# Kernel optimization log

Hardware: AMD Instinct MI355X
Metric: run time of the kernel (lower is better)

The kernel has to match this reference:

```python
import jax, jax.numpy as jnp
import numpy as np

EPS_CB = 1e-6   # ConvBlock norm_layer eps
EPS_LVC = 1e-5  # default BatchNorm2d/1d eps in LVC branch


def _conv(x, w, stride=1, pad=0):
    return jax.lax.conv_general_dilated(
        x, w, (stride, stride), [(pad, pad), (pad, pad)],
        dimension_numbers=("NCHW", "OIHW", "NCHW"))


def _bn2d(x, g, b, eps):
    # inference-style BN with running_mean=0, running_var=1
    inv = 1.0 / jnp.sqrt(1.0 + eps)
    return x * (g * inv)[None, :, None, None] + b[None, :, None, None]


def setup_inputs() -> dict:
    key = jax.random.key(0)
    ks = jax.random.split(key, 24)
    B, C, Cm, K, H, W = 32, 512, 128, 64, 32, 32
    rn = lambda k, s, sc=0.05: jax.random.normal(k, s, dtype=jnp.float32) * sc
    std = 1.0 / (K * C) ** 0.5
    return {
        "x": jax.random.normal(ks[0], (B, C, H, W), dtype=jnp.float32),
        "c1_w": rn(ks[1], (Cm, C, 1, 1)),
        "bn1_g": 1.0 + rn(ks[2], (Cm,)), "bn1_b": rn(ks[3], (Cm,)),
        "c2_w": rn(ks[4], (Cm, Cm, 3, 3)),
        "bn2_g": 1.0 + rn(ks[5], (Cm,)), "bn2_b": rn(ks[6], (Cm,)),
        "c3_w": rn(ks[7], (C, Cm, 1, 1)),
        "bn3_g": 1.0 + rn(ks[8], (C,)), "bn3_b": rn(ks[9], (C,)),
        "rc_w": rn(ks[10], (C, C, 1, 1)),
        "rbn_g": 1.0 + rn(ks[11], (C,)), "rbn_b": rn(ks[12], (C,)),
        "lvc_w": rn(ks[13], (C, C, 1, 1)),
        "lvcbn_g": 1.0 + rn(ks[14], (C,)), "lvcbn_b": rn(ks[15], (C,)),
        "codewords": jax.random.uniform(ks[16], (K, C), minval=-std, maxval=std, dtype=jnp.float32),
        "scale": jax.random.uniform(ks[17], (K,), minval=-1.0, maxval=0.0, dtype=jnp.float32),
        "enbn_g": 1.0 + rn(ks[18], (K,)), "enbn_b": rn(ks[19], (K,)),
        "fc_w": rn(ks[20], (C, C)), "fc_b": rn(ks[21], (C,)),
    }


def reference(x, c1_w, bn1_g, bn1_b, c2_w, bn2_g, bn2_b, c3_w, bn3_g, bn3_b,
              rc_w, rbn_g, rbn_b, lvc_w, lvcbn_g, lvcbn_b,
              codewords, scale, enbn_g, enbn_b, fc_w, fc_b):
    # ---- ConvBlock (ResNet bottleneck with residual 1x1 conv) ----
    h = jax.nn.relu(_bn2d(_conv(x, c1_w), bn1_g, bn1_b, EPS_CB))
    h = jax.nn.relu(_bn2d(_conv(h, c2_w, pad=1), bn2_g, bn2_b, EPS_CB))
    h = _bn2d(_conv(h, c3_w), bn3_g, bn3_b, EPS_CB)
    r = _bn2d(_conv(x, rc_w), rbn_g, rbn_b, EPS_CB)
    xb = jax.nn.relu(h + r)  # (B,C,H,W)

    # ---- LVC: 1x1 conv + BN + ReLU, then Encoding ----
    e = jax.nn.relu(_bn2d(_conv(xb, lvc_w), lvcbn_g, lvcbn_b, EPS_LVC))
    B, C, H, W = e.shape
    ef = e.reshape(B, C, H * W).transpose(0, 2, 1)  # (B,N,C)

    x2 = jnp.sum(ef * ef, axis=-1)                       # (B,N)
    c2 = jnp.sum(codewords * codewords, axis=-1)         # (K,)
    xc = jnp.einsum("bnc,kc->bnk", ef, codewords)        # (B,N,K)
    sl2 = scale[None, None, :] * (x2[:, :, None] - 2.0 * xc + c2[None, None, :])
    a = jax.nn.softmax(sl2, axis=2)                      # (B,N,K)

    # aggregate: sum_n a_{nk} (x_n - c_k)
    enc = jnp.einsum("bnk,bnc->bkc", a, ef) \
          - jnp.sum(a, axis=1)[:, :, None] * codewords[None, :, :]  # (B,K,C)

    # BatchNorm1d over the K (channel) axis, inference-style, then ReLU
    inv = 1.0 / jnp.sqrt(1.0 + EPS_LVC)
    enc = jax.nn.relu(enc * (enbn_g * inv)[None, :, None] + enbn_b[None, :, None])
    en = jnp.mean(enc, axis=1)                           # (B,C)

    # ---- SE-style gating ----
    gam = jax.nn.sigmoid(en @ fc_w.T + fc_b)             # (B,C)
    return jax.nn.relu(xb + xb * gam[:, :, None, None])
```

## Files before the change

### kernel.cpp

```cpp
#include <hip/hip_runtime.h>
#include <math.h>

constexpr int BATCH = 32;
constexpr int C     = 512;
constexpr int CM    = 128;
constexpr int KW    = 64;
constexpr int NPIX  = 1024;

typedef unsigned short u16;
typedef __attribute__((ext_vector_type(8))) short bf16x8;
typedef __attribute__((ext_vector_type(4))) float f32x4;
typedef __attribute__((ext_vector_type(8))) unsigned short u16x8;

__device__ __forceinline__ float bf2f(u16 u) {
    unsigned int v = ((unsigned int)u) << 16;
    return __uint_as_float(v);
}
__device__ __forceinline__ u16 f2bf(float f) {
    unsigned int u = __float_as_uint(f);
    u = u + 0x7FFFu + ((u >> 16) & 1u);
    return (u16)(u >> 16);
}
__device__ __forceinline__ float4 ld4(const float* p) {
    return *reinterpret_cast<const float4*>(p);
}
__device__ __forceinline__ void gload16(const u16* g, u16* l) {
    __builtin_amdgcn_global_load_lds((const __attribute__((address_space(1))) void*)g,
                                     (__attribute__((address_space(3))) void*)l, 16, 0, 0);
}

template<int MODE, int TM, bool RELU>
__global__ __launch_bounds__(256)
void gemm_mfma(const u16* __restrict__ A1, const u16* __restrict__ A2,
               const u16* __restrict__ Wm, u16* __restrict__ outB,
               const float* __restrict__ scale, const float* __restrict__ bias,
               const u16* __restrict__ zbuf, int K, int Cout)
{
    constexpr int MF = TM / 32;
    __shared__ __align__(16) u16 As[TM * 32];
    __shared__ __align__(16) u16 Bs[4096];
    const int b   = blockIdx.z;
    const int n0  = blockIdx.x * TM;
    const int co0 = blockIdx.y * 128;
    const int t    = threadIdx.x;
    const int lane = t & 63;
    const int w    = t >> 6;
    const int wr = w >> 1, wc = w & 1;
    const int lhi = lane >> 4, llo = lane & 15;

    f32x4 acc[MF][4];
#pragma unroll
    for (int i = 0; i < MF; ++i)
#pragma unroll
        for (int j = 0; j < 4; ++j) acc[i][j] = (f32x4){0.f, 0.f, 0.f, 0.f};

    const int aBase = lhi * TM + wr * (TM / 2) + llo;
    const int bBase = lhi * 128 + wc * 64 + llo;

    for (int k0 = 0; k0 < K; k0 += 32) {
#pragma unroll
        for (int rd = 0; rd < (TM * 4) / 256; ++rd) {
            int ch = t + rd * 256;
            int g  = ch / TM, r = ch % TM;
            int kg = k0 + g * 8;
            const u16* src;
            if (MODE == 0) {
                src = A1 + ((size_t)((b << 10) + n0 + r)) * (size_t)K + kg;
            } else if (MODE == 1) {
                int tap = kg >> 7, ci = kg & 127;
                int n = n0 + r;
                int y = (n >> 5) + tap / 3 - 1;
                int x = (n & 31) + tap % 3 - 1;
                src = ((unsigned)y < 32u && (unsigned)x < 32u)
                    ? A1 + ((size_t)((b << 10) + y * 32 + x)) * 128 + ci
                    : zbuf;
            } else {
                src = (kg < 128)
                    ? A1 + ((size_t)((b << 10) + n0 + r)) * 128 + kg
                    : A2 + ((size_t)((b << 10) + n0 + r)) * 512 + (kg - 128);
            }
            gload16(src, &As[ch * 8]);
        }
#pragma unroll
        for (int rd = 0; rd < 2; ++rd) {
            int ch = t + rd * 256;
            int g = ch >> 7, r = ch & 127;
            gload16(Wm + (size_t)(co0 + r) * (size_t)K + k0 + g * 8, &Bs[ch * 8]);
        }
        __syncthreads();
        const bf16x8* Av = (const bf16x8*)As;
        const bf16x8* Bv = (const bf16x8*)Bs;
        bf16x8 af[MF], bfr[4];
#pragma unroll
        for (int m = 0; m < MF; ++m)  af[m]  = Av[aBase + m * 16];
#pragma unroll
        for (int nf = 0; nf < 4; ++nf) bfr[nf] = Bv[bBase + nf * 16];
#pragma unroll
        for (int m = 0; m < MF; ++m)
#pragma unroll
            for (int nf = 0; nf < 4; ++nf)
                acc[m][nf] = __builtin_amdgcn_mfma_f32_16x16x32_bf16(af[m], bfr[nf], acc[m][nf], 0, 0, 0);
        __syncthreads();
    }
#pragma unroll
    for (int nf = 0; nf < 4; ++nf) {
        int coL = co0 + wc * 64 + nf * 16 + llo;
        float s  = scale ? scale[coL] : 1.f;
        float bi = bias  ? bias[coL]  : 0.f;
#pragma unroll
        for (int m = 0; m < MF; ++m) {
            f32x4 v = acc[m][nf];
#pragma unroll
            for (int q = 0; q < 4; ++q) {
                int row = n0 + wr * (TM / 2) + m * 16 + lhi * 4 + q;
                float val = fmaf(v[q], s, bi);
                if (RELU) val = fmaxf(val, 0.f);
                outB[((size_t)((b << 10) + row)) * (size_t)Cout + coL] = f2bf(val);
            }
        }
    }
}

__global__ __launch_bounds__(256)
void gemm_xc(const u16* __restrict__ e, const u16* __restrict__ cwb,
             const float* __restrict__ scale, const float* __restrict__ c2,
             u16* __restrict__ a_t, float* __restrict__ asum)
{
    const int b  = blockIdx.y;
    const int n0 = blockIdx.x * 64;
    const int t    = threadIdx.x;
    const int lane = t & 63;
    const int w    = t >> 6;
    const int wr = w >> 1, wc = w & 1;
    const int lhi = lane >> 4, llo = lane & 15;

    __shared__ __align__(16) char smem[16640];
    u16* As = (u16*)smem;
    u16* Bs = (u16*)(smem + 4096);
    float (*sm)[65] = (float(*)[65])smem;
    __shared__ float x2s[64], pmax[64][4], psum[64][4], sc_s[64], c2_s[64];
    if (t < 64) { sc_s[t] = scale[t]; c2_s[t] = c2[t]; }

    f32x4 acc[2][2];
#pragma unroll
    for (int i = 0; i < 2; ++i)
#pragma unroll
        for (int j = 0; j < 2; ++j) acc[i][j] = (f32x4){0.f, 0.f, 0.f, 0.f};
    float x2p = 0.f;
    const int aBase = lhi * 64 + wr * 32 + llo;
    const int bBase = lhi * 64 + wc * 32 + llo;
    const int xr = w * 16 + (lane >> 2);
    const int xg = lane & 3;

    const int g = t >> 6, r = t & 63;
    for (int k0 = 0; k0 < 512; k0 += 32) {
        gload16(e + ((size_t)((b << 10) + n0 + r)) * 512 + k0 + g * 8, &As[t * 8]);
        gload16(cwb + (size_t)r * 512 + k0 + g * 8, &Bs[t * 8]);
        __syncthreads();
        {
            u16x8 vv = *(const u16x8*)&As[(xg * 64 + xr) * 8];
#pragma unroll
            for (int j = 0; j < 8; ++j) { float f = bf2f(vv[j]); x2p = fmaf(f, f, x2p); }
        }
        const bf16x8* Av = (const bf16x8*)As;
        const bf16x8* Bv = (const bf16x8*)Bs;
        bf16x8 af[2], bfr[2];
#pragma unroll
        for (int m = 0; m < 2; ++m)  af[m]  = Av[aBase + m * 16];
#pragma unroll
        for (int nf = 0; nf < 2; ++nf) bfr[nf] = Bv[bBase + nf * 16];
#pragma unroll
        for (int m = 0; m < 2; ++m)
#pragma unroll
            for (int nf = 0; nf < 2; ++nf)
                acc[m][nf] = __builtin_amdgcn_mfma_f32_16x16x32_bf16(af[m], bfr[nf], acc[m][nf], 0, 0, 0);
        __syncthreads();
    }
    float xs = x2p + __shfl_xor(x2p, 1, 64);
    xs += __shfl_xor(xs, 2, 64);
    if ((lane & 3) == 0) x2s[xr] = xs;
    __syncthreads();
#pragma unroll
    for (int m = 0; m < 2; ++m)
#pragma unroll
        for (int nf = 0; nf < 2; ++nf)
#pragma unroll
            for (int q = 0; q < 4; ++q) {
                int rr = wr * 32 + m * 16 + lhi * 4 + q;
                int cc = wc * 32 + nf * 16 + llo;
                sm[rr][cc] = sc_s[cc] * (x2s[rr] - 2.f * acc[m][nf][q] + c2_s[cc]);
            }
    __syncthreads();
    const int gq = t >> 6;
    float vloc[16];
    float pm = -1e30f;
#pragma unroll
    for (int j = 0; j < 16; ++j) { float v = sm[r][gq * 16 + j]; vloc[j] = v; pm = fmaxf(pm, v); }
    pmax[r][gq] = pm;
    __syncthreads();
    float mm = fmaxf(fmaxf(pmax[r][0], pmax[r][1]), fmaxf(pmax[r][2], pmax[r][3]));
    float ps = 0.f;
#pragma unroll
    for (int j = 0; j < 16; ++j) { float p = __expf(vloc[j] - mm); vloc[j] = p; ps += p; }
    psum[r][gq] = ps;
    __syncthreads();
    float inv = 1.f / (psum[r][0] + psum[r][1] + psum[r][2] + psum[r][3]);
#pragma unroll
    for (int j = 0; j < 16; ++j) {
        int k = gq * 16 + j;
        float av = vloc[j] * inv;
        a_t[((size_t)((b << 6) + k) << 10) + n0 + r] = f2bf(av);
        sm[r][k] = av;
    }
    __syncthreads();
    const int kk = t & 63, rg = t >> 6;
    float pa = 0.f;
#pragma unroll
    for (int j = 0; j < 16; ++j) pa += sm[rg * 16 + j][kk];
    atomicAdd(&asum[(b << 6) + kk], pa);
}

__global__ __launch_bounds__(256)
void enc_mfma(const u16* __restrict__ a_t, const u16* __restrict__ e_t,
              const float* __restrict__ cw, const float* __restrict__ asum,
              const float* __restrict__ sK, const float* __restrict__ bK,
              float* __restrict__ en)
{
    const int b  = blockIdx.y;
    const int c0 = blockIdx.x * 64;
    const int t    = threadIdx.x;
    const int lane = t & 63;
    const int w    = t >> 6;
    const int lhi = lane >> 4, llo = lane & 15;
    __shared__ __align__(16) u16 As[2048];
    __shared__ __align__(16) u16 Bs[2048];
    f32x4 acc[4];
#pragma unroll
    for (int i = 0; i < 4; ++i) acc[i] = (f32x4){0.f, 0.f, 0.f, 0.f};
    const int aBase = lhi * 64 + llo;
    const int bBase = lhi * 64 + w * 16 + llo;
    const int g = t >> 6, r = t & 63;

    for (int n0 = 0; n0 < NPIX; n0 += 32) {
        gload16(a_t + ((size_t)((b << 6) + r) << 10) + n0 + g * 8, &As[t * 8]);
        gload16(e_t + ((size_t)((b << 9) + c0 + r) << 10) + n0 + g * 8, &Bs[t * 8]);
        __syncthreads();
        const bf16x8* Av = (const bf16x8*)As;
        const bf16x8* Bv = (const bf16x8*)Bs;
        bf16x8 bfr = Bv[bBase];
#pragma unroll
        for (int m = 0; m < 4; ++m)
            acc[m] = __builtin_amdgcn_mfma_f32_16x16x32_bf16(Av[aBase + m * 16], bfr, acc[m], 0, 0, 0);
        __syncthreads();
    }
    const int c = c0 + w * 16 + llo;
    float s = 0.f;
#pragma unroll
    for (int m = 0; m < 4; ++m)
#pragma unroll
        for (int q = 0; q < 4; ++q) {
            int k = m * 16 + lhi * 4 + q;
            float v = acc[m][q] - asum[(b << 6) + k] * cw[((size_t)k << 9) + c];
            v = fmaxf(fmaf(v, sK[k], bK[k]), 0.f);
            s += v;
        }
    s += __shfl_xor(s, 16, 64);
    s += __shfl_xor(s, 32, 64);
    if (lane < 16) en[(size_t)(b << 9) + c] = s * (1.f / 64.f);
}

__global__ __launch_bounds__(256)
void tr_in_k(const float* __restrict__ x, u16* __restrict__ xbf)
{
    __shared__ float tile[64][65];
    int b = blockIdx.z, n0 = blockIdx.x * 64, c0 = blockIdx.y * 64, t = threadIdx.x;
#pragma unroll
    for (int q = 0; q < 16; ++q) {
        int idx = t + 256 * q;
        int c = idx >> 6, n = idx & 63;
        tile[c][n] = x[((size_t)((b << 9) + c0 + c) << 10) + n0 + n];
    }
    __syncthreads();
#pragma unroll
    for (int q = 0; q < 16; ++q) {
        int idx = t + 256 * q;
        int nn = idx >> 6, cc = idx & 63;
        xbf[((size_t)((b << 10) + n0 + nn) << 9) + c0 + cc] = f2bf(tile[cc][nn]);
    }
}

__global__ __launch_bounds__(256)
void e_tr_k(const u16* __restrict__ e, u16* __restrict__ e_t)
{
    __shared__ u16 tile[64][65];
    int b = blockIdx.z, n0 = blockIdx.x * 64, c0 = blockIdx.y * 64, t = threadIdx.x;
#pragma unroll
    for (int q = 0; q < 16; ++q) {
        int idx = t + 256 * q;
        int n = idx >> 6, c = idx & 63;
        tile[n][c] = e[((size_t)((b << 10) + n0 + n) << 9) + c0 + c];
    }
    __syncthreads();
#pragma unroll
    for (int q = 0; q < 16; ++q) {
        int idx = t + 256 * q;
        int cc = idx >> 6, nn = idx & 63;
        e_t[((size_t)((b << 9) + c0 + cc) << 10) + n0 + nn] = tile[nn][cc];
    }
}

__global__ __launch_bounds__(256)
void final_tr_k(const u16* __restrict__ xb, const float* __restrict__ gam,
                float* __restrict__ out)
{
    __shared__ float tile[64][65];
    int b = blockIdx.z, n0 = blockIdx.x * 64, c0 = blockIdx.y * 64, t = threadIdx.x;
#pragma unroll
    for (int q = 0; q < 16; ++q) {
        int idx = t + 256 * q;
        int n = idx >> 6, c = idx & 63;
        float gm = 1.f + gam[(b << 9) + c0 + c];
        float v = bf2f(xb[((size_t)((b << 10) + n0 + n) << 9) + c0 + c]) * gm;
        tile[n][c] = fmaxf(v, 0.f);
    }
    __syncthreads();
#pragma unroll
    for (int q = 0; q < 16; ++q) {
        int idx = t + 256 * q;
        int cc = idx >> 6, nn = idx & 63;
        out[((size_t)((b << 9) + c0 + cc) << 10) + n0 + nn] = tile[nn][cc];
    }
}

__global__ __launch_bounds__(256)
void gam_k(const float* __restrict__ en, const float* __restrict__ fcw,
           const float* __restrict__ fcb, float* __restrict__ gam)
{
    int b = blockIdx.x;
    int c = blockIdx.y * 256 + threadIdx.x;
    __shared__ float es[C];
    es[threadIdx.x]       = en[(size_t)b * C + threadIdx.x];
    es[threadIdx.x + 256] = en[(size_t)b * C + threadIdx.x + 256];
    __syncthreads();
    float s = fcb[c];
    const float* wp = fcw + (size_t)c * C;
    for (int i = 0; i < C; i += 4) {
        float4 wv = ld4(wp + i);
        s = fmaf(es[i], wv.x, s);
        s = fmaf(es[i + 1], wv.y, s);
        s = fmaf(es[i + 2], wv.z, s);
        s = fmaf(es[i + 3], wv.w, s);
    }
    gam[(size_t)b * C + c] = 1.f / (1.f + __expf(-s));
}

__global__ __launch_bounds__(256)
void prep_all_k(const float* c1w, const float* bn1g, const float* bn2g,
                const float* c2w, const float* c3w, const float* bn3g,
                const float* bn3b, const float* rcw, const float* rbng,
                const float* rbnb, const float* lvcw, const float* lvcbng,
                const float* enbng, const float* cw,
                u16* c1b, u16* w2b, u16* wcatb, u16* lvcb, u16* cwb,
                float* s1, float* s2, float* slvc, float* bcat,
                float* sK, float* c2, float* asum, u16* zbuf)
{
    const float invCB  = rsqrtf(1.f + 1e-6f);
    const float invLVC = rsqrtf(1.f + 1e-5f);
    long id = (long)blockIdx.x * 256 + threadIdx.x;
    if (id < 327680) {
        int co = (int)(id / 640), k = (int)(id % 640);
        float v = (k < 128) ? c3w[co * 128 + k] * (bn3g[co] * invCB)
                            : rcw[co * 512 + (k - 128)] * (rbng[co] * invCB);
        wcatb[id] = f2bf(v);
        return;
    }
    id -= 327680;
    if (id < 147456) {
        int co = (int)(id / 1152), k = (int)(id % 1152);
        int tap = k >> 7, ci = k & 127;
        w2b[id] = f2bf(c2w[co * 1152 + ci * 9 + tap]);
        return;
    }
    id -= 147456;
    if (id < 262144) { lvcb[id] = f2bf(lvcw[id]); return; }
    id -= 262144;
    if (id < 65536)  { c1b[id]  = f2bf(c1w[id]);  return; }
    id -= 65536;
    if (id < 32768)  { cwb[id]  = f2bf(cw[id]);   return; }
    id -= 32768;
    if (id < 2048)   { asum[id] = 0.f; return; }
    id -= 2048;
    if (id < 1024)   { zbuf[id] = 0;   return; }
    id -= 1024;
    if (id < 128) { s1[id] = bn1g[id] * invCB; return; }
    id -= 128;
    if (id < 128) { s2[id] = bn2g[id] * invCB; return; }
    id -= 128;
    if (id < 512) { slvc[id] = lvcbng[id] * invLVC; return; }
    id -= 512;
    if (id < 512) { bcat[id] = bn3b[id] + rbnb[id]; return; }
    id -= 512;
    if (id < 64)  { sK[id] = enbng[id] * invLVC; return; }
    id -= 64;
    if (id < 64) {
        float s = 0.f;
        for (int c = 0; c < C; ++c) s = fmaf(cw[id * C + c], cw[id * C + c], s);
        c2[id] = s;
    }
}

extern "C" void kernel_launch(void* const* d_in, const int* in_sizes, int n_in,
                              void* d_out, int out_size, void* d_ws, size_t ws_size,
                              hipStream_t stream)
{
    const float* x      = (const float*)d_in[0];
    const float* c1w    = (const float*)d_in[1];
    const float* bn1g   = (const float*)d_in[2];
    const float* bn1b   = (const float*)d_in[3];
    const float* c2w    = (const float*)d_in[4];
    const float* bn2g   = (const float*)d_in[5];
    const float* bn2b   = (const float*)d_in[6];
    const float* c3w    = (const float*)d_in[7];
    const float* bn3g   = (const float*)d_in[8];
    const float* bn3b   = (const float*)d_in[9];
    const float* rcw    = (const float*)d_in[10];
    const float* rbng   = (const float*)d_in[11];
    const float* rbnb   = (const float*)d_in[12];
    const float* lvcw   = (const float*)d_in[13];
    const float* lvcbng = (const float*)d_in[14];
    const float* lvcbnb = (const float*)d_in[15];
    const float* cw     = (const float*)d_in[16];
    const float* scale  = (const float*)d_in[17];
    const float* enbng  = (const float*)d_in[18];
    const float* enbnb  = (const float*)d_in[19];
    const float* fcw    = (const float*)d_in[20];
    const float* fcb    = (const float*)d_in[21];
    float* out = (float*)d_out;
    char* W = (char*)d_ws;

    u16*  xbf  = (u16*)(W);
    u16*  e_b  = xbf;
    u16*  h1   = (u16*)(W + 33554432);
    u16*  a_t  = h1;
    u16*  h2   = (u16*)(W + 41943040);
    u16*  xb_b = (u16*)(W + 50331648);
    u16*  e_t  = (u16*)(W + 83886080);
    char* wb   = W + 117440512;
    u16* c1b   = (u16*)(wb);
    u16* w2b   = (u16*)(wb + 131072);
    u16* wcatb = (u16*)(wb + 425984);
    u16* lvcb  = (u16*)(wb + 1081344);
    u16* cwb   = (u16*)(wb + 1605632);
    float* fb  = (float*)(wb + 1671168);
    float* asum = fb;
    float* en   = fb + 2048;
    float* gam  = fb + 18432;
    float* s1   = fb + 34816;
    float* s2   = s1 + 128;
    float* slvc = s2 + 128;
    float* bcat = slvc + 512;
    float* sK   = bcat + 512;
    float* c2   = sK + 64;
    u16* zbuf   = (u16*)(c2 + 64);

    prep_all_k<<<3282, 256, 0, stream>>>(c1w, bn1g, bn2g, c2w, c3w, bn3g, bn3b,
                                         rcw, rbng, rbnb, lvcw, lvcbng, enbng, cw,
                                         c1b, w2b, wcatb, lvcb, cwb,
                                         s1, s2, slvc, bcat, sK, c2, asum, zbuf);

    tr_in_k<<<dim3(16, 8, 32), 256, 0, stream>>>(x, xbf);

    gemm_mfma<0, 64, true><<<dim3(16, 1, 32), 256, 0, stream>>>(
        xbf, nullptr, c1b, h1, s1, bn1b, zbuf, 512, 128);
    gemm_mfma<1, 64, true><<<dim3(16, 1, 32), 256, 0, stream>>>(
        h1, nullptr, w2b, h2, s2, bn2b, zbuf, 1152, 128);
    gemm_mfma<2, 128, true><<<dim3(8, 4, 32), 256, 0, stream>>>(
        h2, xbf, wcatb, xb_b, nullptr, bcat, zbuf, 640, 512);
    gemm_mfma<0, 128, true><<<dim3(8, 4, 32), 256, 0, stream>>>(
        xb_b, nullptr, lvcb, e_b, slvc, lvcbnb, zbuf, 512, 512);
    e_tr_k<<<dim3(16, 8, 32), 256, 0, stream>>>(e_b, e_t);
    gemm_xc<<<dim3(16, 32), 256, 0, stream>>>(e_b, cwb, scale, c2, a_t, asum);
    enc_mfma<<<dim3(8, 32), 256, 0, stream>>>(a_t, e_t, cw, asum, sK, enbnb, en);
    gam_k<<<dim3(32, 2), 256, 0, stream>>>(en, fcw, fcb, gam);
    final_tr_k<<<dim3(16, 8, 32), 256, 0, stream>>>(xb_b, gam, out);
}
```

Before: 397.9 us.

## Double-buffer GEMM LDS tiles and fuse e transpose into LVC GEMM epilogue

The MFMA GEMM now keeps two LDS buffers and issues the global-to-LDS loads for the next K tile before computing on the current one, which removes one barrier per iteration and hides load latency. The LVC conv GEMM also writes a channel-major transposed copy of its output in the epilogue, so the separate e_tr_k transpose kernel and its extra read of e are removed. Costs: LDS use doubles per block, which may lower occupancy. The epilogue also adds 8-byte strided stores for the transposed output.

```diff
diff --git a/kernel.cpp b/kernel.cpp
--- a/kernel.cpp
+++ b/kernel.cpp
@@ -10,6 +10,7 @@
 typedef unsigned short u16;
 typedef __attribute__((ext_vector_type(8))) short bf16x8;
 typedef __attribute__((ext_vector_type(4))) float f32x4;
+typedef __attribute__((ext_vector_type(4))) unsigned short u16x4;
 typedef __attribute__((ext_vector_type(8))) unsigned short u16x8;
 
 __device__ __forceinline__ float bf2f(u16 u) {
@@ -29,16 +30,17 @@
                                      (__attribute__((address_space(3))) void*)l, 16, 0, 0);
 }
 
-template<int MODE, int TM, bool RELU>
+template<int MODE, int TM, bool RELU, bool WTR>
 __global__ __launch_bounds__(256)
 void gemm_mfma(const u16* __restrict__ A1, const u16* __restrict__ A2,
                const u16* __restrict__ Wm, u16* __restrict__ outB,
+               u16* __restrict__ outT,
                const float* __restrict__ scale, const float* __restrict__ bias,
                const u16* __restrict__ zbuf, int K, int Cout)
 {
     constexpr int MF = TM / 32;
-    __shared__ __align__(16) u16 As[TM * 32];
-    __shared__ __align__(16) u16 Bs[4096];
+    __shared__ __align__(16) u16 As[2][TM * 32];
+    __shared__ __align__(16) u16 Bs[2][4096];
     const int b   = blockIdx.z;
     const int n0  = blockIdx.x * TM;
     const int co0 = blockIdx.y * 128;
@@ -56,8 +58,9 @@
 
     const int aBase = lhi * TM + wr * (TM / 2) + llo;
     const int bBase = lhi * 128 + wc * 64 + llo;
-
-    for (int k0 = 0; k0 < K; k0 += 32) {
+    const int nt = K / 32;
+
+    auto stage = [&](int buf, int k0) {
 #pragma unroll
         for (int rd = 0; rd < (TM * 4) / 256; ++rd) {
             int ch = t + rd * 256;
@@ -79,17 +82,23 @@
                     ? A1 + ((size_t)((b << 10) + n0 + r)) * 128 + kg
                     : A2 + ((size_t)((b << 10) + n0 + r)) * 512 + (kg - 128);
             }
-            gload16(src, &As[ch * 8]);
+            gload16(src, &As[buf][ch * 8]);
         }
 #pragma unroll
         for (int rd = 0; rd < 2; ++rd) {
             int ch = t + rd * 256;
             int g = ch >> 7, r = ch & 127;
-            gload16(Wm + (size_t)(co0 + r) * (size_t)K + k0 + g * 8, &Bs[ch * 8]);
+            gload16(Wm + (size_t)(co0 + r) * (size_t)K + k0 + g * 8, &Bs[buf][ch * 8]);
         }
-        __syncthreads();
-        const bf16x8* Av = (const bf16x8*)As;
-        const bf16x8* Bv = (const bf16x8*)Bs;
+    };
+
+    stage(0, 0);
+    __syncthreads();
+    int cur = 0;
+    for (int ti = 0; ti < nt; ++ti) {
+        if (ti + 1 < nt) stage(cur ^ 1, (ti + 1) * 32);
+        const bf16x8* Av = (const bf16x8*)As[cur];
+        const bf16x8* Bv = (const bf16x8*)Bs[cur];
         bf16x8 af[MF], bfr[4];
 #pragma unroll
         for (int m = 0; m < MF; ++m)  af[m]  = Av[aBase + m * 16];
@@ -101,6 +110,7 @@
             for (int nf = 0; nf < 4; ++nf)
                 acc[m][nf] = __builtin_amdgcn_mfma_f32_16x16x32_bf16(af[m], bfr[nf], acc[m][nf], 0, 0, 0);
         __syncthreads();
+        cur ^= 1;
     }
 #pragma unroll
     for (int nf = 0; nf < 4; ++nf) {
@@ -110,12 +120,19 @@
 #pragma unroll
         for (int m = 0; m < MF; ++m) {
             f32x4 v = acc[m][nf];
+            int rowb = n0 + wr * (TM / 2) + m * 16 + lhi * 4;
+            u16 o[4];
 #pragma unroll
             for (int q = 0; q < 4; ++q) {
-                int row = n0 + wr * (TM / 2) + m * 16 + lhi * 4 + q;
                 float val = fmaf(v[q], s, bi);
                 if (RELU) val = fmaxf(val, 0.f);
-                outB[((size_t)((b << 10) + row)) * (size_t)Cout + coL] = f2bf(val);
+                o[q] = f2bf(val);
+                outB[((size_t)((b << 10) + rowb + q)) * (size_t)Cout + coL] = o[q];
+            }
+            if (WTR) {
+                u16x4 ov;
+                ov[0] = o[0]; ov[1] = o[1]; ov[2] = o[2]; ov[3] = o[3];
+                *(u16x4*)(outT + (((size_t)(b * Cout + coL)) << 10) + rowb) = ov;
             }
         }
     }
@@ -286,26 +303,6 @@
         int idx = t + 256 * q;
         int nn = idx >> 6, cc = idx & 63;
         xbf[((size_t)((b << 10) + n0 + nn) << 9) + c0 + cc] = f2bf(tile[cc][nn]);
-    }
-}
-
-__global__ __launch_bounds__(256)
-void e_tr_k(const u16* __restrict__ e, u16* __restrict__ e_t)
-{
-    __shared__ u16 tile[64][65];
-    int b = blockIdx.z, n0 = blockIdx.x * 64, c0 = blockIdx.y * 64, t = threadIdx.x;
-#pragma unroll
-    for (int q = 0; q < 16; ++q) {
-        int idx = t + 256 * q;
-        int n = idx >> 6, c = idx & 63;
-        tile[n][c] = e[((size_t)((b << 10) + n0 + n) << 9) + c0 + c];
-    }
-    __syncthreads();
-#pragma unroll
-    for (int q = 0; q < 16; ++q) {
-        int idx = t + 256 * q;
-        int cc = idx >> 6, nn = idx & 63;
-        e_t[((size_t)((b << 9) + c0 + cc) << 10) + n0 + nn] = tile[nn][cc];
     }
 }
 
@@ -470,15 +467,14 @@
 
     tr_in_k<<<dim3(16, 8, 32), 256, 0, stream>>>(x, xbf);
 
-    gemm_mfma<0, 64, true><<<dim3(16, 1, 32), 256, 0, stream>>>(
-        xbf, nullptr, c1b, h1, s1, bn1b, zbuf, 512, 128);
-    gemm_mfma<1, 64, true><<<dim3(16, 1, 32), 256, 0, stream>>>(
-        h1, nullptr, w2b, h2, s2, bn2b, zbuf, 1152, 128);
-    gemm_mfma<2, 128, true><<<dim3(8, 4, 32), 256, 0, stream>>>(
-        h2, xbf, wcatb, xb_b, nullptr, bcat, zbuf, 640, 512);
-    gemm_mfma<0, 128, true><<<dim3(8, 4, 32), 256, 0, stream>>>(
-        xb_b, nullptr, lvcb, e_b, slvc, lvcbnb, zbuf, 512, 512);
-    e_tr_k<<<dim3(16, 8, 32), 256, 0, stream>>>(e_b, e_t);
+    gemm_mfma<0, 64, true, false><<<dim3(16, 1, 32), 256, 0, stream>>>(
+        xbf, nullptr, c1b, h1, nullptr, s1, bn1b, zbuf, 512, 128);
+    gemm_mfma<1, 64, true, false><<<dim3(16, 1, 32), 256, 0, stream>>>(
+        h1, nullptr, w2b, h2, nullptr, s2, bn2b, zbuf, 1152, 128);
+    gemm_mfma<2, 128, true, false><<<dim3(8, 4, 32), 256, 0, stream>>>(
+        h2, xbf, wcatb, xb_b, nullptr, nullptr, bcat, zbuf, 640, 512);
+    gemm_mfma<0, 128, true, true><<<dim3(8, 4, 32), 256, 0, stream>>>(
+        xb_b, nullptr, lvcb, e_b, e_t, slvc, lvcbnb, zbuf, 512, 512);
     gemm_xc<<<dim3(16, 32), 256, 0, stream>>>(e_b, cwb, scale, c2, a_t, asum);
     enc_mfma<<<dim3(8, 32), 256, 0, stream>>>(a_t, e_t, cw, asum, sK, enbnb, en);
     gam_k<<<dim3(32, 2), 256, 0, stream>>>(en, fcw, fcb, gam);
```

New measurement: 385.2 us. 1.03x faster.
